# Optimization experiments

Measured on AMD Instinct MI355X. Metric: run time of the kernel, lower is better.

Reference implementation:

```python
import jax, jax.numpy as jnp
import numpy as np

N = 65536      # total agents
A = 49152
E = 786432     # edges in active subgraph (avg degree 16)
H = 64         # hidden_dim
L = 3          # num GAT layers
NEG_SLOPE = 0.2
LN_EPS = 1e-5


def setup_inputs() -> dict:
    rng = np.random.default_rng(0)
    arrivals = jnp.asarray(rng.uniform(0.0, 25.0, N).astype(np.float32))
    departures = arrivals + jnp.asarray(rng.uniform(10.0, 60.0, N).astype(np.float32))
    is_hard = jnp.asarray(rng.integers(0, 2, N).astype(np.float32))
    masked_indices = jnp.asarray(np.sort(rng.choice(N, A, replace=False)).astype(np.int32))
    edge_index = jnp.asarray(rng.integers(0, A, (2, E)).astype(np.int32))

    def w(*shape):
        return jnp.asarray((rng.standard_normal(shape) * 0.05).astype(np.float32))

    return {
        'arrivals': arrivals, 'departures': departures, 'is_hard': is_hard,
        'masked_indices': masked_indices, 'edge_index': edge_index, 'timestep': 30,
        'W_emb1': w(2, H), 'b_emb1': jnp.zeros((H,), jnp.float32),
        'W_emb2': w(H, H), 'b_emb2': jnp.zeros((H,), jnp.float32),
        'lin_W': w(L, H, H), 'att_src': w(L, H), 'att_dst': w(L, H),
        'gat_bias': jnp.zeros((L, H), jnp.float32),
        'select_W': w(H, 1), 'select_b': jnp.zeros((1,), jnp.float32),
    }


def reference(arrivals, departures, is_hard, masked_indices, edge_index, timestep,
              W_emb1, b_emb1, W_emb2, b_emb2, lin_W, att_src, att_dst, gat_bias,
              select_W, select_b):
    nA = masked_indices.shape[0]
    # gather active-node features, build 2-dim input (progress, hard-to-match)
    arr = arrivals[masked_indices]
    dep = departures[masked_indices]
    progress = (timestep - arr) / (dep - arr)
    feat = jnp.stack([progress, is_hard[masked_indices]], axis=1)  # [A, 2]

    # embedding: two stacked Linear layers (no nonlinearity, as in the source)
    x = (feat @ W_emb1 + b_emb1) @ W_emb2 + b_emb2                 # [A, H]

    # edge list with self-loops appended (GATConv add_self_loops=True)
    loop = jnp.arange(nA, dtype=edge_index.dtype)
    src = jnp.concatenate([edge_index[0], loop])
    dst = jnp.concatenate([edge_index[1], loop])

    # GAT stack (heads=1, ReLU between layers, none after last)
    h = x
    for l in range(L):
        hw = h @ lin_W[l]                                          # [A, H]
        a_s = hw @ att_src[l]                                      # [A]
        a_d = hw @ att_dst[l]                                      # [A]
        e = a_s[src] + a_d[dst]                                    # [E+A]
        e = jnp.where(e > 0, e, NEG_SLOPE * e)                     # leaky_relu
        # segment softmax over incoming edges per destination node
        m = jax.ops.segment_max(e, dst, num_segments=nA)
        ee = jnp.exp(e - m[dst])
        denom = jax.ops.segment_sum(ee, dst, num_segments=nA)
        alpha = ee / denom[dst]
        h = jax.ops.segment_sum(hw[src] * alpha[:, None], dst, num_segments=nA)
        h = h + gat_bias[l]
        if l < L - 1:
            h = jax.nn.relu(h)

    x = x + h
    # F.layer_norm over last dim, no affine params
    mu = jnp.mean(x, axis=-1, keepdims=True)
    var = jnp.mean((x - mu) ** 2, axis=-1, keepdims=True)
    x = (x - mu) / jnp.sqrt(var + LN_EPS)

    x = jax.nn.sigmoid(x @ select_W + select_b)                    # [A, 1]

    # scatter scores back into full node tensor
    ret = jnp.zeros((arrivals.shape[0], 1), x.dtype).at[masked_indices].set(x)
    return ret
```

## Files before the change

### kernel.cpp

```cpp
#include <hip/hip_runtime.h>
#include <math.h>

#define HDIM 64
#define NEG 0.2f
#define LN_EPS 1e-5f
#define NBK_SHIFT 8
#define CAP 5120
#define EPB 2048
#define LIN_BLOCKS 768

static __device__ __forceinline__ float wred_sum(float v){
  #pragma unroll
  for (int d = 32; d >= 1; d >>= 1) v += __shfl_xor(v, d, 64);
  return v;
}
static __device__ __forceinline__ float wred_max(float v){
  #pragma unroll
  for (int d = 32; d >= 1; d >>= 1) v = fmaxf(v, __shfl_xor(v, d, 64));
  return v;
}
static __device__ __forceinline__ int wscan_incl_i(int v){
  #pragma unroll
  for (int d = 1; d < 64; d <<= 1){
    int t = __shfl_up(v, d, 64);
    if ((int)(threadIdx.x & 63) >= d) v += t;
  }
  return v;
}
static __device__ __forceinline__ float b2f(unsigned short u){
  union { unsigned u; float f; } x; x.u = ((unsigned)u) << 16; return x.f;
}
static __device__ __forceinline__ unsigned short f2b(float f){
  unsigned u = __float_as_uint(f);
  return (unsigned short)((u + 0x7FFF + ((u >> 16) & 1)) >> 16);
}

__global__ void precompute_emb(const float* __restrict__ W1, const float* __restrict__ b1,
                               const float* __restrict__ W2, const float* __restrict__ b2,
                               float* __restrict__ Wc, float* __restrict__ bc){
  int k = threadIdx.x;
  float c0 = 0.f, c1 = 0.f, cb = 0.f;
  for (int j = 0; j < HDIM; j++){
    float w2 = W2[j*HDIM + k];
    c0 += W1[j]        * w2;
    c1 += W1[HDIM + j] * w2;
    cb += b1[j]        * w2;
  }
  Wc[k] = c0; Wc[HDIM + k] = c1; bc[k] = cb + b2[k];
}

__global__ void __launch_bounds__(256) embed_kernel(
    const float* __restrict__ arrivals, const float* __restrict__ departures,
    const float* __restrict__ is_hard, const int* __restrict__ masked,
    const int* __restrict__ timestep,
    const float* __restrict__ Wc, const float* __restrict__ bc,
    float* __restrict__ x_emb, int nA,
    int* __restrict__ bcursor, int nbk, float* __restrict__ outz, int outN){
  int idx = blockIdx.x*256 + threadIdx.x;
  if (idx < nbk) bcursor[idx] = idx * CAP;
  if (idx < outN) outz[idx] = 0.f;
  int lane = threadIdx.x & 63;
  int i = (blockIdx.x << 2) | (threadIdx.x >> 6);
  i = __builtin_amdgcn_readfirstlane(i);
  if (i >= nA) return;
  int   mi  = masked[i];
  float ts  = (float)timestep[0];
  float arr = arrivals[mi];
  float dep = departures[mi];
  float hrd = is_hard[mi];
  float p   = (ts - arr) / (dep - arr);
  float x   = fmaf(p, Wc[lane], fmaf(hrd, Wc[HDIM + lane], bc[lane]));
  x_emb[i*HDIM + lane] = x;
}

__global__ void __launch_bounds__(256) bucket_bin(
    const int* __restrict__ src, const int* __restrict__ dst,
    int* __restrict__ bcursor, int* __restrict__ pairs, int E, int nbk){
  extern __shared__ int lds[];
  int* hist  = lds;
  int* gbase = lds + nbk;
  int t = threadIdx.x;
  for (int i = t; i < nbk; i += 256) hist[i] = 0;
  __syncthreads();
  int e0 = blockIdx.x * EPB;
  int s[8], d[8];
  #pragma unroll
  for (int j = 0; j < 8; j++){
    int e = e0 + j*256 + t;
    if (e < E){
      s[j] = src[e]; d[j] = dst[e];
      atomicAdd(&hist[d[j] >> NBK_SHIFT], 1);
    } else d[j] = -1;
  }
  __syncthreads();
  for (int i = t; i < nbk; i += 256){
    int h = hist[i];
    gbase[i] = h ? atomicAdd(&bcursor[i], h) : 0;
    hist[i] = 0;
  }
  __syncthreads();
  #pragma unroll
  for (int j = 0; j < 8; j++){
    if (d[j] >= 0){
      int b = d[j] >> NBK_SHIFT;
      int lp = atomicAdd(&hist[b], 1);
      int pos = gbase[b] + lp;
      if (pos < (b + 1) * CAP)
        pairs[pos] = s[j] | ((d[j] & 255) << 16);
    }
  }
}

#define PPT 20
__global__ void __launch_bounds__(256) bucket_expand(
    const int* __restrict__ pairs, const int* __restrict__ bcursor,
    int* __restrict__ ssrc, int* __restrict__ offs, int* __restrict__ ends, int nA){
  __shared__ int hist[256];
  __shared__ int wsums[4];
  __shared__ int lcur[256];
  int t = threadIdx.x, lane = t & 63, w = t >> 6;
  int b = blockIdx.x;
  int base = b * CAP;
  int used = bcursor[b] - base;
  if (used > CAP) used = CAP;
  hist[t] = 0;
  __syncthreads();
  int myP[PPT];
  #pragma unroll
  for (int j = 0; j < PPT; j++){
    int i = t + j*256;
    myP[j] = (i < used) ? pairs[base + i] : -1;
  }
  #pragma unroll
  for (int j = 0; j < PPT; j++)
    if (myP[j] != -1) atomicAdd(&hist[(unsigned)myP[j] >> 16], 1);
  __syncthreads();
  int cnt = hist[t];
  int incl = wscan_incl_i(cnt);
  if (lane == 63) wsums[w] = incl;
  __syncthreads();
  int wexcl = 0;
  #pragma unroll
  for (int k = 0; k < 4; k++) if (k < w) wexcl += wsums[k];
  int off_d = base + wexcl + (incl - cnt);
  int g = (b << NBK_SHIFT) + t;
  if (g < nA){ offs[g] = off_d; ends[g] = off_d + cnt; }
  lcur[t] = off_d;
  __syncthreads();
  #pragma unroll
  for (int j = 0; j < PPT; j++){
    if (myP[j] != -1){
      int pos = atomicAdd(&lcur[(unsigned)myP[j] >> 16], 1);
      ssrc[pos] = myP[j] & 0xFFFF;
    }
  }
}

__global__ void __launch_bounds__(256) gat_linear(
    const float* __restrict__ hin, const float* __restrict__ W,
    const float* __restrict__ att_s, const float* __restrict__ att_d,
    unsigned short* __restrict__ hw16, float* __restrict__ a_s, float* __restrict__ a_d,
    int nA, int totalWaves){
  int lane = threadIdx.x & 63;
  int w = threadIdx.x >> 6;
  float Wreg[HDIM];
  #pragma unroll
  for (int k = 0; k < HDIM; k++) Wreg[k] = W[k*HDIM + lane];
  float asl = att_s[lane], adl = att_d[lane];
  int waveId = blockIdx.x*4 + w;
  for (int row0 = waveId; row0 < nA; row0 += totalWaves){
    int row = __builtin_amdgcn_readfirstlane(row0);
    const float* hrow = hin + (size_t)row*HDIM;
    float acc0 = 0.f, acc1 = 0.f, acc2 = 0.f, acc3 = 0.f;
    #pragma unroll
    for (int k = 0; k < HDIM; k += 4){
      float4 h4 = *(const float4*)(hrow + k);
      acc0 = fmaf(h4.x, Wreg[k],   acc0);
      acc1 = fmaf(h4.y, Wreg[k+1], acc1);
      acc2 = fmaf(h4.z, Wreg[k+2], acc2);
      acc3 = fmaf(h4.w, Wreg[k+3], acc3);
    }
    float acc = (acc0 + acc1) + (acc2 + acc3);
    hw16[(size_t)row*HDIM + lane] = f2b(acc);
    float vs = wred_sum(acc * asl);
    float vd = wred_sum(acc * adl);
    if (lane == 0){ a_s[row] = vs; a_d[row] = vd; }
  }
}

__global__ void __launch_bounds__(256) gat_aggregate(
    const unsigned short* __restrict__ hw16,
    const float* __restrict__ a_s, const float* __restrict__ a_d,
    const int* __restrict__ offs, const int* __restrict__ ends,
    const int* __restrict__ srcs, const float* __restrict__ bias,
    float* __restrict__ hout, int nA, int doRelu, int doFinal,
    const float* __restrict__ x_emb, const float* __restrict__ selW,
    const float* __restrict__ selb, const int* __restrict__ masked,
    float* __restrict__ out){
  int lane = threadIdx.x & 63;
  int i = (blockIdx.x << 2) | (threadIdx.x >> 6);
  i = __builtin_amdgcn_readfirstlane(i);
  if (i >= nA) return;
  int off = offs[i], end = ends[i];
  float adi = a_d[i];
  float es = a_s[i] + adi; es = es > 0.f ? es : NEG*es;
  float m = es, denom = 1.f;
  float acc0 = b2f(hw16[(size_t)i*HDIM + lane]);
  float acc1 = 0.f, acc2 = 0.f, acc3 = 0.f;
  for (int cbase = off; cbase < end; cbase += 64){
    int cnt = end - cbase; if (cnt > 64) cnt = 64;
    int   s = 0; float e = -3.4e38f;
    if (lane < cnt){
      s = srcs[cbase + lane];
      e = a_s[s] + adi;
      e = e > 0.f ? e : NEG*e;
    }
    float cm = wred_max(e);
    if (cm > m){
      float scale = __expf(m - cm);
      denom *= scale; m = cm;
      acc0 *= scale; acc1 *= scale; acc2 *= scale; acc3 *= scale;
    }
    float p = (lane < cnt) ? __expf(e - m) : 0.f;
    denom += wred_sum(p);
    int cnt4 = (cnt + 3) & ~3;
    for (int tt = 0; tt < cnt4; tt += 4){
      int   sj0 = __builtin_amdgcn_readfirstlane(__shfl(s, tt,   64));
      int   sj1 = __builtin_amdgcn_readfirstlane(__shfl(s, tt+1, 64));
      int   sj2 = __builtin_amdgcn_readfirstlane(__shfl(s, tt+2, 64));
      int   sj3 = __builtin_amdgcn_readfirstlane(__shfl(s, tt+3, 64));
      float pj0 = __shfl(p, tt,   64), pj1 = __shfl(p, tt+1, 64);
      float pj2 = __shfl(p, tt+2, 64), pj3 = __shfl(p, tt+3, 64);
      float v0 = b2f(hw16[(size_t)sj0*HDIM + lane]);
      float v1 = b2f(hw16[(size_t)sj1*HDIM + lane]);
      float v2 = b2f(hw16[(size_t)sj2*HDIM + lane]);
      float v3 = b2f(hw16[(size_t)sj3*HDIM + lane]);
      acc0 = fmaf(pj0, v0, acc0);
      acc1 = fmaf(pj1, v1, acc1);
      acc2 = fmaf(pj2, v2, acc2);
      acc3 = fmaf(pj3, v3, acc3);
    }
  }
  float acc = (acc0 + acc1) + (acc2 + acc3);
  float r = acc/denom + bias[lane];
  if (doFinal){
    float x  = x_emb[(size_t)i*HDIM + lane] + r;
    float mu = wred_sum(x) * (1.f/HDIM);
    float dd = x - mu;
    float var = wred_sum(dd*dd) * (1.f/HDIM);
    float xn  = dd / sqrtf(var + LN_EPS);
    float dot = wred_sum(xn * selW[lane]);
    if (lane == 0){
      float z = dot + selb[0];
      out[masked[i]] = 1.f / (1.f + __expf(-z));
    }
  } else {
    if (doRelu) r = fmaxf(r, 0.f);
    hout[(size_t)i*HDIM + lane] = r;
  }
}

extern "C" void kernel_launch(void* const* d_in, const int* in_sizes, int n_in,
                              void* d_out, int out_size, void* d_ws, size_t ws_size,
                              hipStream_t stream) {
  const float* arrivals   = (const float*)d_in[0];
  const float* departures = (const float*)d_in[1];
  const float* is_hard    = (const float*)d_in[2];
  const int*   masked     = (const int*)  d_in[3];
  const int*   edge_index = (const int*)  d_in[4];
  const int*   timestep   = (const int*)  d_in[5];
  const float* W_emb1     = (const float*)d_in[6];
  const float* b_emb1     = (const float*)d_in[7];
  const float* W_emb2     = (const float*)d_in[8];
  const float* b_emb2     = (const float*)d_in[9];
  const float* lin_W      = (const float*)d_in[10];
  const float* att_src    = (const float*)d_in[11];
  const float* att_dst    = (const float*)d_in[12];
  const float* gat_bias   = (const float*)d_in[13];
  const float* select_W   = (const float*)d_in[14];
  const float* select_b   = (const float*)d_in[15];

  int nA = in_sizes[3];
  int E  = in_sizes[4] / 2;
  const int* esrc = edge_index;
  const int* edst = edge_index + E;
  int nbk = (nA + (1 << NBK_SHIFT) - 1) >> NBK_SHIFT;

  char* ws = (char*)d_ws;
  size_t o = 0;
  auto alloc = [&](size_t bytes) -> void* {
    void* p = ws + o; o += (bytes + 255) & ~(size_t)255; return p;
  };
  float*          x_emb   = (float*)alloc((size_t)nA*HDIM*sizeof(float));
  float*          hbuf    = (float*)alloc((size_t)nA*HDIM*sizeof(float));
  unsigned short* hw16    = (unsigned short*)alloc((size_t)nA*HDIM*sizeof(unsigned short));
  float*          asb     = (float*)alloc((size_t)nA*sizeof(float));
  float*          adb     = (float*)alloc((size_t)nA*sizeof(float));
  float*          Wc      = (float*)alloc(2*HDIM*sizeof(float));
  float*          bc      = (float*)alloc(HDIM*sizeof(float));
  int*            offs    = (int*)  alloc((size_t)nA*sizeof(int));
  int*            ends    = (int*)  alloc((size_t)nA*sizeof(int));
  int*            bcursor = (int*)  alloc((size_t)(nbk+4)*sizeof(int));
  int*            ssrc    = (int*)  alloc((size_t)nbk*CAP*sizeof(int));
  int*            pairs   = (int*)hw16;

  precompute_emb<<<1, 64, 0, stream>>>(W_emb1, b_emb1, W_emb2, b_emb2, Wc, bc);

  int rowBlocks = (nA + 3) / 4;
  embed_kernel<<<rowBlocks, 256, 0, stream>>>(arrivals, departures, is_hard, masked,
                                              timestep, Wc, bc, x_emb, nA,
                                              bcursor, nbk, (float*)d_out, out_size);
  int binBlocks = (E + EPB - 1) / EPB;
  bucket_bin<<<binBlocks, 256, 2*nbk*sizeof(int), stream>>>(esrc, edst, bcursor, pairs, E, nbk);
  bucket_expand<<<nbk, 256, 0, stream>>>(pairs, bcursor, ssrc, offs, ends, nA);

  const float* hin = x_emb;
  int totalWaves = LIN_BLOCKS * 4;
  for (int l = 0; l < 3; l++){
    gat_linear<<<LIN_BLOCKS, 256, 0, stream>>>(hin, lin_W + (size_t)l*HDIM*HDIM,
                                               att_src + l*HDIM, att_dst + l*HDIM,
                                               hw16, asb, adb, nA, totalWaves);
    gat_aggregate<<<rowBlocks, 256, 0, stream>>>(hw16, asb, adb, offs, ends, ssrc,
                                                 gat_bias + l*HDIM, hbuf, nA,
                                                 (l < 2) ? 1 : 0, (l == 2) ? 1 : 0,
                                                 x_emb, select_W, select_b, masked,
                                                 (float*)d_out);
    hin = hbuf;
  }
}
```

Measured before the change: 297.2 us.

## Split wave into four 16-lane groups gathering neighbor rows with 8-byte loads

The GAT aggregation kernel now splits each 64-lane wave into four 16-lane groups. Each group loads a whole 128-byte bf16 neighbor row as ushort4 per lane, so a wave processes 8 neighbors per iteration instead of 4 with 2-byte loads per lane. Partial accumulators are combined across groups with xor shuffles, and the epilogue (bias, ReLU, layernorm and select) is vectorized with float4. This is meant to issue fewer, wider memory instructions and drop the scalar readfirstlane serialization. In exchange it adds cross-group reductions, pads neighbor counts to multiples of 8, and relies on 32-bit byte-offset arithmetic.

```diff
diff --git a/kernel.cpp b/kernel.cpp
--- a/kernel.cpp
+++ b/kernel.cpp
@@ -198,6 +198,8 @@
     const float* __restrict__ selb, const int* __restrict__ masked,
     float* __restrict__ out){
   int lane = threadIdx.x & 63;
+  int grp  = lane >> 4;
+  int gl   = lane & 15;
   int i = (blockIdx.x << 2) | (threadIdx.x >> 6);
   i = __builtin_amdgcn_readfirstlane(i);
   if (i >= nA) return;
@@ -205,8 +207,11 @@
   float adi = a_d[i];
   float es = a_s[i] + adi; es = es > 0.f ? es : NEG*es;
   float m = es, denom = 1.f;
-  float acc0 = b2f(hw16[(size_t)i*HDIM + lane]);
-  float acc1 = 0.f, acc2 = 0.f, acc3 = 0.f;
+  float a0=0.f,a1=0.f,a2=0.f,a3=0.f, c0=0.f,c1=0.f,c2=0.f,c3=0.f;
+  if (grp == 0){
+    ushort4 sv = *(const ushort4*)(hw16 + (size_t)i*HDIM + gl*4);
+    a0 = b2f(sv.x); a1 = b2f(sv.y); a2 = b2f(sv.z); a3 = b2f(sv.w);
+  }
   for (int cbase = off; cbase < end; cbase += 64){
     int cnt = end - cbase; if (cnt > 64) cnt = 64;
     int   s = 0; float e = -3.4e38f;
@@ -217,46 +222,63 @@
     }
     float cm = wred_max(e);
     if (cm > m){
-      float scale = __expf(m - cm);
-      denom *= scale; m = cm;
-      acc0 *= scale; acc1 *= scale; acc2 *= scale; acc3 *= scale;
+      float sc = __expf(m - cm);
+      denom *= sc; m = cm;
+      a0*=sc; a1*=sc; a2*=sc; a3*=sc; c0*=sc; c1*=sc; c2*=sc; c3*=sc;
     }
     float p = (lane < cnt) ? __expf(e - m) : 0.f;
     denom += wred_sum(p);
-    int cnt4 = (cnt + 3) & ~3;
-    for (int tt = 0; tt < cnt4; tt += 4){
-      int   sj0 = __builtin_amdgcn_readfirstlane(__shfl(s, tt,   64));
-      int   sj1 = __builtin_amdgcn_readfirstlane(__shfl(s, tt+1, 64));
-      int   sj2 = __builtin_amdgcn_readfirstlane(__shfl(s, tt+2, 64));
-      int   sj3 = __builtin_amdgcn_readfirstlane(__shfl(s, tt+3, 64));
-      float pj0 = __shfl(p, tt,   64), pj1 = __shfl(p, tt+1, 64);
-      float pj2 = __shfl(p, tt+2, 64), pj3 = __shfl(p, tt+3, 64);
-      float v0 = b2f(hw16[(size_t)sj0*HDIM + lane]);
-      float v1 = b2f(hw16[(size_t)sj1*HDIM + lane]);
-      float v2 = b2f(hw16[(size_t)sj2*HDIM + lane]);
-      float v3 = b2f(hw16[(size_t)sj3*HDIM + lane]);
-      acc0 = fmaf(pj0, v0, acc0);
-      acc1 = fmaf(pj1, v1, acc1);
-      acc2 = fmaf(pj2, v2, acc2);
-      acc3 = fmaf(pj3, v3, acc3);
-    }
-  }
-  float acc = (acc0 + acc1) + (acc2 + acc3);
-  float r = acc/denom + bias[lane];
+    int cnt8 = (cnt + 7) & ~7;
+    for (int tt = 0; tt < cnt8; tt += 8){
+      int   sjA = __shfl(s, tt + grp,     64);
+      float pjA = __shfl(p, tt + grp,     64);
+      int   sjB = __shfl(s, tt + 4 + grp, 64);
+      float pjB = __shfl(p, tt + 4 + grp, 64);
+      unsigned oA = ((unsigned)sjA << 7) | (gl << 3);
+      unsigned oB = ((unsigned)sjB << 7) | (gl << 3);
+      ushort4 vA = *(const ushort4*)((const char*)hw16 + oA);
+      ushort4 vB = *(const ushort4*)((const char*)hw16 + oB);
+      a0 = fmaf(pjA, b2f(vA.x), a0);
+      a1 = fmaf(pjA, b2f(vA.y), a1);
+      a2 = fmaf(pjA, b2f(vA.z), a2);
+      a3 = fmaf(pjA, b2f(vA.w), a3);
+      c0 = fmaf(pjB, b2f(vB.x), c0);
+      c1 = fmaf(pjB, b2f(vB.y), c1);
+      c2 = fmaf(pjB, b2f(vB.z), c2);
+      c3 = fmaf(pjB, b2f(vB.w), c3);
+    }
+  }
+  a0 += c0; a1 += c1; a2 += c2; a3 += c3;
+  a0 += __shfl_xor(a0, 16, 64); a0 += __shfl_xor(a0, 32, 64);
+  a1 += __shfl_xor(a1, 16, 64); a1 += __shfl_xor(a1, 32, 64);
+  a2 += __shfl_xor(a2, 16, 64); a2 += __shfl_xor(a2, 32, 64);
+  a3 += __shfl_xor(a3, 16, 64); a3 += __shfl_xor(a3, 32, 64);
+  float inv = 1.f / denom;
+  float4 b4 = *(const float4*)(bias + gl*4);
+  float r0 = fmaf(a0, inv, b4.x);
+  float r1 = fmaf(a1, inv, b4.y);
+  float r2 = fmaf(a2, inv, b4.z);
+  float r3 = fmaf(a3, inv, b4.w);
   if (doFinal){
-    float x  = x_emb[(size_t)i*HDIM + lane] + r;
-    float mu = wred_sum(x) * (1.f/HDIM);
-    float dd = x - mu;
-    float var = wred_sum(dd*dd) * (1.f/HDIM);
-    float xn  = dd / sqrtf(var + LN_EPS);
-    float dot = wred_sum(xn * selW[lane]);
+    float4 xe = *(const float4*)(x_emb + (size_t)i*HDIM + gl*4);
+    float x0 = xe.x + r0, x1 = xe.y + r1, x2 = xe.z + r2, x3 = xe.w + r3;
+    float mu  = wred_sum(x0 + x1 + x2 + x3) * (1.f/(HDIM*4));
+    float d0 = x0-mu, d1 = x1-mu, d2 = x2-mu, d3 = x3-mu;
+    float var = wred_sum(d0*d0 + d1*d1 + d2*d2 + d3*d3) * (1.f/(HDIM*4));
+    float rstd = 1.f / sqrtf(var + LN_EPS);
+    float4 w4 = *(const float4*)(selW + gl*4);
+    float dot = wred_sum((d0*w4.x + d1*w4.y + d2*w4.z + d3*w4.w) * rstd) * 0.25f;
     if (lane == 0){
       float z = dot + selb[0];
       out[masked[i]] = 1.f / (1.f + __expf(-z));
     }
   } else {
-    if (doRelu) r = fmaxf(r, 0.f);
-    hout[(size_t)i*HDIM + lane] = r;
+    if (doRelu){
+      r0 = fmaxf(r0, 0.f); r1 = fmaxf(r1, 0.f);
+      r2 = fmaxf(r2, 0.f); r3 = fmaxf(r3, 0.f);
+    }
+    if (grp == 0)
+      *(float4*)(hout + (size_t)i*HDIM + gl*4) = make_float4(r0, r1, r2, r3);
   }
 }
 
```

Result: faster. 276.6 us (-6.9%).
